# Performance work log

Hardware: AMD Instinct MI355X
Metric: run time of the kernel (lower is better)

The kernel has to match this reference:

```python
import jax, jax.numpy as jnp
import numpy as np

B, L, D = 2, 2048, 1024
H = 16          # num_heads
HD = D // H     # head_dim = 64
NEG_INF = jnp.float32(-1e30)


def setup_inputs() -> dict:
    key = jax.random.key(0)
    ks = jax.random.split(key, 10)
    s = 1.0 / np.sqrt(D)
    return {
        "x": jax.random.normal(ks[0], (B, L, D), dtype=jnp.float32),
        "Wq": jax.random.normal(ks[1], (D, D), dtype=jnp.float32) * s,
        "bq": jnp.zeros((D,), jnp.float32),
        "Wk": jax.random.normal(ks[2], (D, D), dtype=jnp.float32) * s,
        "bk": jnp.zeros((D,), jnp.float32),
        "Wv": jax.random.normal(ks[3], (D, D), dtype=jnp.float32) * s,
        "bv": jnp.zeros((D,), jnp.float32),
        "Wo": jax.random.normal(ks[4], (D, D), dtype=jnp.float32) * s,
        "bo": jnp.zeros((D,), jnp.float32),
        "local_scale": jnp.ones((1,), jnp.float32),
        "global_scale": jnp.ones((1,), jnp.float32),
    }


def reference(x, Wq, bq, Wk, bk, Wv, bv, Wo, bo, local_scale, global_scale):
    # projections -> [B, H, L, HD]
    def proj(W, b):
        return (x @ W + b).reshape(B, L, H, HD).transpose(0, 2, 1, 3)
    Q, K, V = proj(Wq, bq), proj(Wk, bk), proj(Wv, bv)
    lh = H // 2
    inv_sqrt = 1.0 / jnp.sqrt(jnp.float32(HD))

    # local (causal) heads
    scores_l = jnp.einsum("bhqd,bhkd->bhqk", Q[:, :lh], K[:, :lh]) * inv_sqrt
    causal = jnp.tril(jnp.ones((L, L), dtype=bool))  # keep lower triangle
    scores_l = jnp.where(causal, scores_l * local_scale, NEG_INF)
    attn_local = jax.nn.softmax(scores_l, axis=-1)
    out_local = jnp.einsum("bhqk,bhkd->bhqd", attn_local, V[:, :lh])

    # global (full) heads
    scores_g = jnp.einsum("bhqd,bhkd->bhqk", Q[:, lh:], K[:, lh:]) * inv_sqrt
    attn_global = jax.nn.softmax(scores_g * global_scale, axis=-1)
    out_global = jnp.einsum("bhqk,bhkd->bhqd", attn_global, V[:, lh:])

    out = jnp.concatenate([out_local, out_global], axis=1)  # [B,H,L,HD]
    out = out.transpose(0, 2, 1, 3).reshape(B, L, D)
    out = out @ Wo + bo
    return (out, attn_local, attn_global)
```

## Files before the change

### kernel.cpp

```cpp
#include <hip/hip_runtime.h>
#include <hip/hip_bf16.h>

#define B 2
#define L 2048
#define D 1024
#define H 16
#define HD 64
#define LH 8
#define NEG_INF -1e30f

typedef __hip_bfloat16 bf16;
typedef unsigned short ushort_t;
typedef short bf16x8 __attribute__((ext_vector_type(8)));
typedef unsigned short us8 __attribute__((ext_vector_type(8)));
typedef float f32x4 __attribute__((ext_vector_type(4)));

#define MFMA16(a, b, c) __builtin_amdgcn_mfma_f32_16x16x32_bf16((a), (b), (c), 0, 0, 0)

#if defined(__has_builtin)
#if __has_builtin(__builtin_amdgcn_global_load_lds)
#define HAVE_GLOAD_LDS 1
#endif
#endif

template<typename T> struct IsF32;
template<> struct IsF32<float> { static constexpr int value = 1; };
template<> struct IsF32<bf16>  { static constexpr int value = 0; };

__device__ __forceinline__ float ldf(const float* p, size_t i) { return p[i]; }
__device__ __forceinline__ float ldf(const bf16* p, size_t i) { return __bfloat162float(p[i]); }

__device__ __forceinline__ float4 ld4(const float* p, size_t i) {
  return *reinterpret_cast<const float4*>(p + i);
}
__device__ __forceinline__ float4 ld4(const bf16* p, size_t i) {
  ushort4 u = *reinterpret_cast<const ushort4*>(p + i);
  float4 f;
  f.x = __uint_as_float(((unsigned)u.x) << 16);
  f.y = __uint_as_float(((unsigned)u.y) << 16);
  f.z = __uint_as_float(((unsigned)u.z) << 16);
  f.w = __uint_as_float(((unsigned)u.w) << 16);
  return f;
}
__device__ __forceinline__ ushort_t bfh(float v) {
  bf16 h = __float2bfloat16(v);
  return *reinterpret_cast<ushort_t*>(&h);
}
__device__ __forceinline__ float bf2f(ushort_t u) {
  return __uint_as_float(((unsigned)u) << 16);
}
__device__ __forceinline__ void stf(float* p, size_t i, float v) { p[i] = v; }
__device__ __forceinline__ void stf(bf16* p, size_t i, float v) { p[i] = __float2bfloat16(v); }

__device__ __forceinline__ int swz(int row, int slot) {
  return row * 64 + (((slot ^ (row & 7)) & 7) << 3);
}
__device__ __forceinline__ int swzc(int row, int c) {
  return row * 64 + (((((c >> 3) ^ row) & 7) << 3) | (c & 7));
}

#if defined(HAVE_GLOAD_LDS)
__device__ __forceinline__ void gload_lds16(const ushort_t* src, ushort_t* dst) {
  __builtin_amdgcn_global_load_lds(
      (const __attribute__((address_space(1))) unsigned int*)src,
      (__attribute__((address_space(3))) unsigned int*)dst, 16, 0, 0);
}
#endif

__device__ __forceinline__ void stage64(const ushort_t* g, size_t gstride,
                                        ushort_t* lds, int w, int ln) {
  #pragma unroll
  for (int c = 0; c < 2; ++c) {
    const int row = 16 * w + 8 * c + (ln >> 3);
    const int slot = ((ln & 7) ^ row) & 7;
    const ushort_t* src = g + (size_t)row * gstride + slot * 8;
#if defined(HAVE_GLOAD_LDS)
    gload_lds16(src, lds + (size_t)(16 * w + 8 * c) * 64);
#else
    *reinterpret_cast<uint4*>(&lds[row * 64 + (ln & 7) * 8]) =
        *reinterpret_cast<const uint4*>(src);
#endif
  }
}

__device__ __forceinline__ void stage128(const ushort_t* g, ushort_t* lds,
                                         int w, int ln) {
  #pragma unroll
  for (int c = 0; c < 4; ++c) {
    const int row = 32 * w + 8 * c + (ln >> 3);
    const int slot = ((ln & 7) ^ row) & 7;
    const ushort_t* src = g + (size_t)row * 1024 + slot * 8;
#if defined(HAVE_GLOAD_LDS)
    gload_lds16(src, lds + (size_t)(32 * w + 8 * c) * 64);
#else
    *reinterpret_cast<uint4*>(&lds[row * 64 + (ln & 7) * 8]) =
        *reinterpret_cast<const uint4*>(src);
#endif
  }
}

__global__ void detect_dtype_kernel(const unsigned short* __restrict__ x,
                                    int* __restrict__ flag) {
  int bad = 0;
  for (int i = threadIdx.x; i < 1024; i += 64) {
    if (((x[i] >> 7) & 0xFF) >= 170) bad = 1;
  }
  unsigned long long m = __ballot(bad);
  if (threadIdx.x == 0) *flag = (m != 0ULL) ? 1 : 0;
}

__global__ __launch_bounds__(256)
void split_f32_kernel(const int* __restrict__ flag, int want,
                      const float* __restrict__ in,
                      ushort_t* __restrict__ hp, ushort_t* __restrict__ lp, int n4) {
  if (*flag != want) return;
  int i = blockIdx.x * 256 + threadIdx.x;
  const int stride = gridDim.x * 256;
  for (; i < n4; i += stride) {
    float4 v = *reinterpret_cast<const float4*>(in + 4 * (size_t)i);
    ushort4 h, l;
    h.x = bfh(v.x); l.x = bfh(v.x - bf2f(h.x));
    h.y = bfh(v.y); l.y = bfh(v.y - bf2f(h.y));
    h.z = bfh(v.z); l.z = bfh(v.z - bf2f(h.z));
    h.w = bfh(v.w); l.w = bfh(v.w - bf2f(h.w));
    *reinterpret_cast<ushort4*>(hp + 4 * (size_t)i) = h;
    *reinterpret_cast<ushort4*>(lp + 4 * (size_t)i) = l;
  }
}

template<typename T>
__global__ __launch_bounds__(256)
void transW_kernel(const int* __restrict__ flag,
                   const T* __restrict__ W0, const T* __restrict__ W1,
                   const T* __restrict__ W2, const T* __restrict__ W3,
                   ushort_t* __restrict__ base, ushort_t* __restrict__ baseWo,
                   int lo_upto) {
  if (*flag != IsF32<T>::value) return;
  const int z = blockIdx.z;
  const T* W = z == 0 ? W0 : (z == 1 ? W1 : (z == 2 ? W2 : W3));
  ushort_t* hp = (z < 3) ? (base + (size_t)z * 2097152) : baseWo;
  ushort_t* lp = hp + 1048576;
  const bool wl_ = IsF32<T>::value && (z < lo_upto);
  __shared__ float ts[64][69];
  const int k0 = blockIdx.x * 64, n0 = blockIdx.y * 64;
  const int t = threadIdx.x;
  #pragma unroll
  for (int p = 0; p < 4; ++p) {
    int r = p * 16 + (t >> 4);
    int c = (t & 15) * 4;
    float4 v = ld4(W, (size_t)(k0 + r) * D + n0 + c);
    ts[r][c] = v.x; ts[r][c + 1] = v.y; ts[r][c + 2] = v.z; ts[r][c + 3] = v.w;
  }
  __syncthreads();
  #pragma unroll
  for (int p = 0; p < 4; ++p) {
    int n = p * 16 + (t >> 4);
    int k4 = (t & 15) * 4;
    ushort4 h, l;
    float a0 = ts[k4][n], a1 = ts[k4 + 1][n], a2 = ts[k4 + 2][n], a3 = ts[k4 + 3][n];
    h.x = bfh(a0); l.x = bfh(a0 - bf2f(h.x));
    h.y = bfh(a1); l.y = bfh(a1 - bf2f(h.y));
    h.z = bfh(a2); l.z = bfh(a2 - bf2f(h.z));
    h.w = bfh(a3); l.w = bfh(a3 - bf2f(h.w));
    size_t o = (size_t)(n0 + n) * D + k0 + k4;
    *reinterpret_cast<ushort4*>(hp + o) = h;
    if (wl_) *reinterpret_cast<ushort4*>(lp + o) = l;
  }
}

template<typename T, int NSA, bool FULL>
__global__ __launch_bounds__(256, FULL ? 3 : 4)
void gemm_kernel(const int* __restrict__ flag,
                 const ushort_t* __restrict__ xA, const ushort_t* __restrict__ xAl,
                 const ushort_t* __restrict__ aoh,
                 const ushort_t* __restrict__ wbase, const ushort_t* __restrict__ woT,
                 const T* __restrict__ bq, const T* __restrict__ bk,
                 const T* __restrict__ bv, const T* __restrict__ bo,
                 ushort_t* __restrict__ qh, ushort_t* __restrict__ ql,
                 ushort_t* __restrict__ kh, ushort_t* __restrict__ kl,
                 ushort_t* __restrict__ vth, T* __restrict__ out0, int zfix) {
  if (*flag != IsF32<T>::value) return;
  const int cpx = gridDim.x >> 3;
  const int swzid = ((int)blockIdx.x & 7) * cpx + ((int)blockIdx.x >> 3);
  const int mtile = swzid & 31;
  const int ntile = (swzid >> 5) & 15;
  const int z = (zfix >= 0) ? zfix : (swzid >> 9);
  const int m0 = mtile * 128, n0 = ntile * 64;

  const bool isOut = (z == 3);
  const ushort_t* Ah = isOut ? aoh : xA;
  const ushort_t* wh = isOut ? woT : (wbase + (size_t)z * 2097152);
  const ushort_t* wl = wh + 1048576;

  constexpr int LDSUS = FULL ? 24576 : 12288;
  __shared__ ushort_t lds[LDSUS];
  ushort_t* AsH = lds;
  ushort_t* BsH = lds + 8192;
  ushort_t* AsL = FULL ? (lds + 12288) : nullptr;
  ushort_t* BsL = FULL ? (lds + 20480) : nullptr;

  const int ln = threadIdx.x & 63, w = threadIdx.x >> 6;
  const int m = ln & 15, hi = ln >> 4;

  f32x4 acc[2][4] = {};

  for (int k0 = 0; k0 < 1024; k0 += 64) {
    stage128(Ah + (size_t)m0 * 1024 + k0, AsH, w, ln);
    stage64(wh + (size_t)n0 * 1024 + k0, 1024, BsH, w, ln);
    if constexpr (FULL) {
      stage128(xAl + (size_t)m0 * 1024 + k0, AsL, w, ln);
      stage64(wl + (size_t)n0 * 1024 + k0, 1024, BsL, w, ln);
    }
    __syncthreads();
    #pragma unroll
    for (int kc = 0; kc < 2; ++kc) {
      bf16x8 a_h[2], b_h[4];
      #pragma unroll
      for (int f = 0; f < 2; ++f)
        a_h[f] = *reinterpret_cast<const bf16x8*>(&AsH[swz(w * 32 + f * 16 + m, kc * 4 + hi)]);
      #pragma unroll
      for (int f = 0; f < 4; ++f)
        b_h[f] = *reinterpret_cast<const bf16x8*>(&BsH[swz(f * 16 + m, kc * 4 + hi)]);
      #pragma unroll
      for (int fr = 0; fr < 2; ++fr)
        #pragma unroll
        for (int fc = 0; fc < 4; ++fc)
          acc[fr][fc] = MFMA16(a_h[fr], b_h[fc], acc[fr][fc]);
      if constexpr (FULL) {
        bf16x8 a_l[2], b_l[4];
        #pragma unroll
        for (int f = 0; f < 2; ++f)
          a_l[f] = *reinterpret_cast<const bf16x8*>(&AsL[swz(w * 32 + f * 16 + m, kc * 4 + hi)]);
        #pragma unroll
        for (int f = 0; f < 4; ++f)
          b_l[f] = *reinterpret_cast<const bf16x8*>(&BsL[swz(f * 16 + m, kc * 4 + hi)]);
        #pragma unroll
        for (int fr = 0; fr < 2; ++fr)
          #pragma unroll
          for (int fc = 0; fc < 4; ++fc) {
            acc[fr][fc] = MFMA16(a_h[fr], b_l[fc], acc[fr][fc]);
            acc[fr][fc] = MFMA16(a_l[fr], b_h[fc], acc[fr][fc]);
          }
      }
    }
    __syncthreads();
  }

  #pragma unroll
  for (int fc = 0; fc < 4; ++fc) {
    const int col = n0 + fc * 16 + m;
    if (isOut) {
      const float bv_ = ldf(bo, (size_t)col);
      #pragma unroll
      for (int fr = 0; fr < 2; ++fr)
        #pragma unroll
        for (int r = 0; r < 4; ++r) {
          const int tok = m0 + w * 32 + fr * 16 + 4 * hi + r;
          stf(out0, (size_t)tok * D + col, acc[fr][fc][r] + bv_);
        }
    } else if (z == 2) {
      const int hh = col >> 6, d = col & 63;
      const float bv_ = ldf(bv, (size_t)col);
      #pragma unroll
      for (int fr = 0; fr < 2; ++fr) {
        const int tok0 = m0 + w * 32 + fr * 16 + 4 * hi;
        const int bb = tok0 >> 11, ll = tok0 & (L - 1);
        ushort4 hv;
        hv.x = bfh(acc[fr][fc][0] + bv_);
        hv.y = bfh(acc[fr][fc][1] + bv_);
        hv.z = bfh(acc[fr][fc][2] + bv_);
        hv.w = bfh(acc[fr][fc][3] + bv_);
        *reinterpret_cast<ushort4*>(
            &vth[((size_t)(bb * H + hh) * HD + d) * L + ll]) = hv;
      }
    } else {
      const int hh = col >> 6, d = col & 63;
      const float bv_ = ldf(z == 0 ? bq : bk, (size_t)col);
      ushort_t* oh = z == 0 ? qh : kh;
      ushort_t* ol = z == 0 ? ql : kl;
      #pragma unroll
      for (int fr = 0; fr < 2; ++fr)
        #pragma unroll
        for (int r = 0; r < 4; ++r) {
          const int tok = m0 + w * 32 + fr * 16 + 4 * hi + r;
          const int bb = tok >> 11, ll = tok & (L - 1);
          const float v = acc[fr][fc][r] + bv_;
          const size_t o = ((size_t)(bb * H + hh) * L + ll) * HD + d;
          const ushort_t hu = bfh(v);
          oh[o] = hu; ol[o] = bfh(v - bf2f(hu));
        }
    }
  }
}

template<typename T>
__global__ __launch_bounds__(256, 2)
void attn_kernel(const int* __restrict__ flag,
                 const ushort_t* __restrict__ Qh_g, const ushort_t* __restrict__ Ql_g,
                 const ushort_t* __restrict__ Kh_g, const ushort_t* __restrict__ Kl_g,
                 const ushort_t* __restrict__ Vth_g,
                 const T* __restrict__ lsp, const T* __restrict__ gsp,
                 T* __restrict__ attn_l, T* __restrict__ attn_g,
                 ushort_t* __restrict__ AOh) {
  if (*flag != IsF32<T>::value) return;
  const int bid = blockIdx.x;
  const int xcd = bid & 7, slot = bid >> 3;
  const int bhg = xcd + 8 * (slot >> 5);
  const int strip_raw = slot & 31;
  const int bb = bhg >> 4, h = bhg & 15;
  const bool is_local = h < LH;
  const int strip = is_local ? (31 - strip_raw) : strip_raw;
  const int q0 = strip * 64;
  const int ln = threadIdx.x & 63, w = threadIdx.x >> 6;
  const int m = ln & 15, hi = ln >> 4;

  const float cscale =
      (is_local ? ldf(lsp, (size_t)0) : ldf(gsp, (size_t)0)) * 0.125f;
  const size_t bh_off = ((size_t)bb * H + h) * L * HD;
  const ushort_t* Qhb = Qh_g + bh_off;
  const ushort_t* Qlb = Ql_g + bh_off;
  const ushort_t* Khb = Kh_g + bh_off;
  const ushort_t* Klb = Kl_g + bh_off;
  const ushort_t* Vhb = Vth_g + bh_off;

  __shared__ ushort_t KsH[2][4096], KsL[2][4096], VsH[2][4096], Ps[4096];

  bf16x8 qfh[2], qfl[2];
  {
    const size_t qb = (size_t)(q0 + 16 * w + m) * HD + hi * 8;
    qfh[0] = *reinterpret_cast<const bf16x8*>(Qhb + qb);
    qfh[1] = *reinterpret_cast<const bf16x8*>(Qhb + qb + 32);
    qfl[0] = *reinterpret_cast<const bf16x8*>(Qlb + qb);
    qfl[1] = *reinterpret_cast<const bf16x8*>(Qlb + qb + 32);
  }

  float m_ = NEG_INF, l_ = 0.f;
  const int nkt = is_local ? (strip + 1) : (L / 64);
  T* aout = is_local ? attn_l : attn_g;
  const size_t arow0 =
      ((size_t)(bb * LH + (is_local ? h : h - LH)) * L + q0) * L;

  stage64(Khb, HD, KsH[0], w, ln);
  __syncthreads();
  for (int kt = 0; kt < nkt; ++kt) {
    const int cur = kt & 1;
    if (kt + 1 < nkt)
      stage64(Khb + (size_t)((kt + 1) * 64) * HD, HD, KsH[cur ^ 1], w, ln);

    f32x4 s[4] = {};
    __builtin_amdgcn_s_setprio(1);
    #pragma unroll
    for (int nt = 0; nt < 4; ++nt) {
      #pragma unroll
      for (int kc = 0; kc < 2; ++kc) {
        bf16x8 kbh = *reinterpret_cast<const bf16x8*>(&KsH[cur][swz(nt * 16 + m, kc * 4 + hi)]);
        s[nt] = MFMA16(kbh, qfh[kc], s[nt]);
      }
    }
    __builtin_amdgcn_s_setprio(0);

    const bool dg = is_local && (kt == strip);
    #pragma unroll
    for (int nt = 0; nt < 4; ++nt)
      #pragma unroll
      for (int r = 0; r < 4; ++r) {
        float v = s[nt][r] * cscale;
        if (dg && (nt * 16 + 4 * hi + r > 16 * w + m)) v = NEG_INF;
        s[nt][r] = v;
      }

    float tm = NEG_INF;
    #pragma unroll
    for (int nt = 0; nt < 4; ++nt)
      #pragma unroll
      for (int r = 0; r < 4; ++r) tm = fmaxf(tm, s[nt][r]);
    tm = fmaxf(tm, __shfl_xor(tm, 16, 64));
    tm = fmaxf(tm, __shfl_xor(tm, 32, 64));
    const float mn = fmaxf(m_, tm);
    float sum = 0.f;
    #pragma unroll
    for (int nt = 0; nt < 4; ++nt)
      #pragma unroll
      for (int r = 0; r < 4; ++r) sum += __expf(s[nt][r] - mn);
    sum += __shfl_xor(sum, 16, 64);
    sum += __shfl_xor(sum, 32, 64);
    l_ = l_ * __expf(m_ - mn) + sum;
    m_ = mn;
    __syncthreads();
  }

  const float invl = 1.0f / l_;
  f32x4 o_[4] = {};

  stage64(Khb, HD, KsH[0], w, ln);
  stage64(Klb, HD, KsL[0], w, ln);
  stage64(Vhb, L, VsH[0], w, ln);
  __syncthreads();
  for (int kt = 0; kt < nkt; ++kt) {
    const int cur = kt & 1;
    if (kt + 1 < nkt) {
      stage64(Khb + (size_t)((kt + 1) * 64) * HD, HD, KsH[cur ^ 1], w, ln);
      stage64(Klb + (size_t)((kt + 1) * 64) * HD, HD, KsL[cur ^ 1], w, ln);
      stage64(Vhb + (size_t)((kt + 1) * 64), L, VsH[cur ^ 1], w, ln);
    }

    f32x4 s[4] = {};
    __builtin_amdgcn_s_setprio(1);
    #pragma unroll
    for (int nt = 0; nt < 4; ++nt) {
      #pragma unroll
      for (int kc = 0; kc < 2; ++kc) {
        bf16x8 kbh = *reinterpret_cast<const bf16x8*>(&KsH[cur][swz(nt * 16 + m, kc * 4 + hi)]);
        bf16x8 kbl = *reinterpret_cast<const bf16x8*>(&KsL[cur][swz(nt * 16 + m, kc * 4 + hi)]);
        s[nt] = MFMA16(kbh, qfh[kc], s[nt]);
        s[nt] = MFMA16(kbl, qfh[kc], s[nt]);
        s[nt] = MFMA16(kbh, qfl[kc], s[nt]);
      }
    }
    __builtin_amdgcn_s_setprio(0);

    const bool dg = is_local && (kt == strip);
    #pragma unroll
    for (int nt = 0; nt < 4; ++nt) {
      float v0 = s[nt][0] * cscale, v1 = s[nt][1] * cscale;
      float v2 = s[nt][2] * cscale, v3 = s[nt][3] * cscale;
      if (dg) {
        const int kbq = nt * 16 + 4 * hi, qq = 16 * w + m;
        if (kbq + 0 > qq) v0 = NEG_INF;
        if (kbq + 1 > qq) v1 = NEG_INF;
        if (kbq + 2 > qq) v2 = NEG_INF;
        if (kbq + 3 > qq) v3 = NEG_INF;
      }
      ushort4 pk;
      pk.x = bfh(__expf(v0 - m_) * invl);
      pk.y = bfh(__expf(v1 - m_) * invl);
      pk.z = bfh(__expf(v2 - m_) * invl);
      pk.w = bfh(__expf(v3 - m_) * invl);
      *reinterpret_cast<ushort4*>(&Ps[swzc(16 * w + m, nt * 16 + 4 * hi)]) = pk;
    }

    __builtin_amdgcn_s_setprio(1);
    bf16x8 pf0 = *reinterpret_cast<const bf16x8*>(&Ps[swz(16 * w + m, hi)]);
    bf16x8 pf1 = *reinterpret_cast<const bf16x8*>(&Ps[swz(16 * w + m, 4 + hi)]);
    #pragma unroll
    for (int dt = 0; dt < 4; ++dt) {
      bf16x8 vf0 = *reinterpret_cast<const bf16x8*>(&VsH[cur][swz(dt * 16 + m, hi)]);
      bf16x8 vf1 = *reinterpret_cast<const bf16x8*>(&VsH[cur][swz(dt * 16 + m, 4 + hi)]);
      o_[dt] = MFMA16(pf0, vf0, o_[dt]);
      o_[dt] = MFMA16(pf1, vf1, o_[dt]);
    }
    __builtin_amdgcn_s_setprio(0);

    {
      const int pr = 16 * w + (ln >> 2);
      const int cs = (ln & 3) * 2;
      us8 v0 = *reinterpret_cast<const us8*>(&Ps[swz(pr, cs)]);
      us8 v1 = *reinterpret_cast<const us8*>(&Ps[swz(pr, cs + 1)]);
      const size_t gi = arow0 + (size_t)pr * L + (size_t)(kt * 64 + (ln & 3) * 16);
      if constexpr (IsF32<T>::value) {
        float* dst = (float*)aout + gi;
        *reinterpret_cast<float4*>(dst + 0) =
            make_float4(bf2f(v0[0]), bf2f(v0[1]), bf2f(v0[2]), bf2f(v0[3]));
        *reinterpret_cast<float4*>(dst + 4) =
            make_float4(bf2f(v0[4]), bf2f(v0[5]), bf2f(v0[6]), bf2f(v0[7]));
        *reinterpret_cast<float4*>(dst + 8) =
            make_float4(bf2f(v1[0]), bf2f(v1[1]), bf2f(v1[2]), bf2f(v1[3]));
        *reinterpret_cast<float4*>(dst + 12) =
            make_float4(bf2f(v1[4]), bf2f(v1[5]), bf2f(v1[6]), bf2f(v1[7]));
      } else {
        bf16* dst = (bf16*)aout + gi;
        *reinterpret_cast<uint4*>(dst + 0) = *reinterpret_cast<const uint4*>(&v0);
        *reinterpret_cast<uint4*>(dst + 8) = *reinterpret_cast<const uint4*>(&v1);
      }
    }
    __syncthreads();
  }

  if (is_local) {
    const int pr = 16 * w + (ln >> 2);
    const size_t rbase = arow0 + (size_t)pr * L;
    for (int c = nkt * 64 + (ln & 3) * 16; c < L; c += 64) {
      if constexpr (IsF32<T>::value) {
        float* dst = (float*)aout + rbase + c;
        const float4 z4 = make_float4(0.f, 0.f, 0.f, 0.f);
        *reinterpret_cast<float4*>(dst + 0) = z4;
        *reinterpret_cast<float4*>(dst + 4) = z4;
        *reinterpret_cast<float4*>(dst + 8) = z4;
        *reinterpret_cast<float4*>(dst + 12) = z4;
      } else {
        bf16* dst = (bf16*)aout + rbase + c;
        const uint4 z4 = make_uint4(0u, 0u, 0u, 0u);
        *reinterpret_cast<uint4*>(dst + 0) = z4;
        *reinterpret_cast<uint4*>(dst + 8) = z4;
      }
    }
  }

  #pragma unroll
  for (int dt = 0; dt < 4; ++dt)
    #pragma unroll
    for (int r = 0; r < 4; ++r)
      AOh[((size_t)bb * L + q0 + 16 * w + 4 * hi + r) * D + h * HD + dt * 16 + m] =
          bfh(o_[dt][r]);
}

template<typename T>
static void launch_path(void* const* d_in, void* d_out, void* d_ws, hipStream_t stream) {
  const int want = IsF32<T>::value;
  const int* flag = (const int*)d_ws;
  ushort_t* Qh  = (ushort_t*)((char*)d_ws + 256);
  ushort_t* Ql  = Qh + 4194304;
  ushort_t* Kh  = Ql + 4194304;
  ushort_t* Kl  = Kh + 4194304;
  ushort_t* Vth = Kl + 4194304;
  ushort_t* AOh = Vth + 4194304;
  ushort_t* Woth = AOh + 4194304;

  const T* x  = (const T*)d_in[0];
  const T* Wq = (const T*)d_in[1];
  const T* bq = (const T*)d_in[2];
  const T* Wk = (const T*)d_in[3];
  const T* bk = (const T*)d_in[4];
  const T* Wv = (const T*)d_in[5];
  const T* bv = (const T*)d_in[6];
  const T* Wo = (const T*)d_in[7];
  const T* bo = (const T*)d_in[8];
  const T* ls = (const T*)d_in[9];
  const T* gs = (const T*)d_in[10];

  T* out0   = (T*)d_out;
  T* attn_l = out0 + (size_t)B * L * D;
  T* attn_g = attn_l + (size_t)B * LH * L * L;
  ushort_t* xh  = (ushort_t*)attn_g;
  ushort_t* xl  = xh + 4194304;
  ushort_t* Wt3 = xh + 8388608;

  constexpr int NSA = IsF32<T>::value ? 2 : 1;

  if constexpr (IsF32<T>::value)
    split_f32_kernel<<<1024, 256, 0, stream>>>(flag, want, (const float*)x, xh, xl, 1048576);
  transW_kernel<T><<<dim3(16, 16, 4), 256, 0, stream>>>(
      flag, Wq, Wk, Wv, Wo, Wt3, Woth, 2);
  const ushort_t* xA = IsF32<T>::value ? xh : (const ushort_t*)x;

  if constexpr (IsF32<T>::value) {
    gemm_kernel<T, NSA, true><<<1024, 256, 0, stream>>>(
        flag, xA, xl, AOh, Wt3, Woth, bq, bk, bv, bo,
        Qh, Ql, Kh, Kl, Vth, out0, -1);
    gemm_kernel<T, NSA, false><<<512, 256, 0, stream>>>(
        flag, xA, xl, AOh, Wt3, Woth, bq, bk, bv, bo,
        Qh, Ql, Kh, Kl, Vth, out0, 2);
  } else {
    gemm_kernel<T, NSA, false><<<1536, 256, 0, stream>>>(
        flag, xA, xl, AOh, Wt3, Woth, bq, bk, bv, bo,
        Qh, Ql, Kh, Kl, Vth, out0, -1);
  }
  attn_kernel<T><<<1024, 256, 0, stream>>>(
      flag, Qh, Ql, Kh, Kl, Vth, ls, gs, attn_l, attn_g, AOh);
  gemm_kernel<T, NSA, false><<<512, 256, 0, stream>>>(
      flag, xA, xl, AOh, Wt3, Woth, bq, bk, bv, bo,
      Qh, Ql, Kh, Kl, Vth, out0, 3);
}

extern "C" void kernel_launch(void* const* d_in, const int* in_sizes, int n_in,
                              void* d_out, int out_size, void* d_ws, size_t ws_size,
                              hipStream_t stream) {
  int* flag = (int*)d_ws;
  detect_dtype_kernel<<<1, 64, 0, stream>>>((const unsigned short*)d_in[0], flag);
  launch_path<float>(d_in, d_out, d_ws, stream);
  launch_path<bf16>(d_in, d_out, d_ws, stream);
}
```

Baseline: 966.9 us.

## Drop split-bf16 precision in projections, double-buffer GEMM, single-buffer V in attention

Removes the hi/lo bf16 split of x and the Q/K weights, so the Q/K projection GEMMs run a single bf16 MFMA pass and all projections use one unified GEMM launch. The GEMM k-loop gains double-buffered LDS staging with raised MFMA wave priority. The attention kernel single-buffers V with an extra barrier, freeing LDS so occupancy can rise to 3 blocks. The trade-off is lower projection accuracy for Q/K, which could affect attention-probability tolerance, and the V load is no longer prefetched.

Result: faster. 927.3 us (-4.1%).

```diff
diff --git a/kernel.cpp b/kernel.cpp
--- a/kernel.cpp
+++ b/kernel.cpp
@@ -110,21 +110,17 @@
 }
 
 __global__ __launch_bounds__(256)
-void split_f32_kernel(const int* __restrict__ flag, int want,
-                      const float* __restrict__ in,
-                      ushort_t* __restrict__ hp, ushort_t* __restrict__ lp, int n4) {
+void cast_f32_kernel(const int* __restrict__ flag, int want,
+                     const float* __restrict__ in,
+                     ushort_t* __restrict__ hp, int n4) {
   if (*flag != want) return;
   int i = blockIdx.x * 256 + threadIdx.x;
   const int stride = gridDim.x * 256;
   for (; i < n4; i += stride) {
     float4 v = *reinterpret_cast<const float4*>(in + 4 * (size_t)i);
-    ushort4 h, l;
-    h.x = bfh(v.x); l.x = bfh(v.x - bf2f(h.x));
-    h.y = bfh(v.y); l.y = bfh(v.y - bf2f(h.y));
-    h.z = bfh(v.z); l.z = bfh(v.z - bf2f(h.z));
-    h.w = bfh(v.w); l.w = bfh(v.w - bf2f(h.w));
+    ushort4 h;
+    h.x = bfh(v.x); h.y = bfh(v.y); h.z = bfh(v.z); h.w = bfh(v.w);
     *reinterpret_cast<ushort4*>(hp + 4 * (size_t)i) = h;
-    *reinterpret_cast<ushort4*>(lp + 4 * (size_t)i) = l;
   }
 }
 
@@ -133,14 +129,11 @@
 void transW_kernel(const int* __restrict__ flag,
                    const T* __restrict__ W0, const T* __restrict__ W1,
                    const T* __restrict__ W2, const T* __restrict__ W3,
-                   ushort_t* __restrict__ base, ushort_t* __restrict__ baseWo,
-                   int lo_upto) {
+                   ushort_t* __restrict__ base, ushort_t* __restrict__ baseWo) {
   if (*flag != IsF32<T>::value) return;
   const int z = blockIdx.z;
   const T* W = z == 0 ? W0 : (z == 1 ? W1 : (z == 2 ? W2 : W3));
   ushort_t* hp = (z < 3) ? (base + (size_t)z * 2097152) : baseWo;
-  ushort_t* lp = hp + 1048576;
-  const bool wl_ = IsF32<T>::value && (z < lo_upto);
   __shared__ float ts[64][69];
   const int k0 = blockIdx.x * 64, n0 = blockIdx.y * 64;
   const int t = threadIdx.x;
@@ -156,23 +149,19 @@
   for (int p = 0; p < 4; ++p) {
     int n = p * 16 + (t >> 4);
     int k4 = (t & 15) * 4;
-    ushort4 h, l;
-    float a0 = ts[k4][n], a1 = ts[k4 + 1][n], a2 = ts[k4 + 2][n], a3 = ts[k4 + 3][n];
-    h.x = bfh(a0); l.x = bfh(a0 - bf2f(h.x));
-    h.y = bfh(a1); l.y = bfh(a1 - bf2f(h.y));
-    h.z = bfh(a2); l.z = bfh(a2 - bf2f(h.z));
-    h.w = bfh(a3); l.w = bfh(a3 - bf2f(h.w));
-    size_t o = (size_t)(n0 + n) * D + k0 + k4;
-    *reinterpret_cast<ushort4*>(hp + o) = h;
-    if (wl_) *reinterpret_cast<ushort4*>(lp + o) = l;
-  }
-}
-
-template<typename T, int NSA, bool FULL>
-__global__ __launch_bounds__(256, FULL ? 3 : 4)
+    ushort4 h;
+    h.x = bfh(ts[k4][n]);
+    h.y = bfh(ts[k4 + 1][n]);
+    h.z = bfh(ts[k4 + 2][n]);
+    h.w = bfh(ts[k4 + 3][n]);
+    *reinterpret_cast<ushort4*>(&hp[(size_t)(n0 + n) * D + k0 + k4]) = h;
+  }
+}
+
+template<typename T>
+__global__ __launch_bounds__(256, 3)
 void gemm_kernel(const int* __restrict__ flag,
-                 const ushort_t* __restrict__ xA, const ushort_t* __restrict__ xAl,
-                 const ushort_t* __restrict__ aoh,
+                 const ushort_t* __restrict__ xA, const ushort_t* __restrict__ aoh,
                  const ushort_t* __restrict__ wbase, const ushort_t* __restrict__ woT,
                  const T* __restrict__ bq, const T* __restrict__ bk,
                  const T* __restrict__ bv, const T* __restrict__ bo,
@@ -190,59 +179,40 @@
   const bool isOut = (z == 3);
   const ushort_t* Ah = isOut ? aoh : xA;
   const ushort_t* wh = isOut ? woT : (wbase + (size_t)z * 2097152);
-  const ushort_t* wl = wh + 1048576;
-
-  constexpr int LDSUS = FULL ? 24576 : 12288;
-  __shared__ ushort_t lds[LDSUS];
-  ushort_t* AsH = lds;
-  ushort_t* BsH = lds + 8192;
-  ushort_t* AsL = FULL ? (lds + 12288) : nullptr;
-  ushort_t* BsL = FULL ? (lds + 20480) : nullptr;
+
+  __shared__ ushort_t As[2][8192], Bs[2][4096];
 
   const int ln = threadIdx.x & 63, w = threadIdx.x >> 6;
   const int m = ln & 15, hi = ln >> 4;
 
   f32x4 acc[2][4] = {};
 
-  for (int k0 = 0; k0 < 1024; k0 += 64) {
-    stage128(Ah + (size_t)m0 * 1024 + k0, AsH, w, ln);
-    stage64(wh + (size_t)n0 * 1024 + k0, 1024, BsH, w, ln);
-    if constexpr (FULL) {
-      stage128(xAl + (size_t)m0 * 1024 + k0, AsL, w, ln);
-      stage64(wl + (size_t)n0 * 1024 + k0, 1024, BsL, w, ln);
-    }
-    __syncthreads();
+  stage128(Ah + (size_t)m0 * 1024, As[0], w, ln);
+  stage64(wh + (size_t)n0 * 1024, 1024, Bs[0], w, ln);
+  __syncthreads();
+  for (int step = 0; step < 16; ++step) {
+    const int cur = step & 1;
+    if (step < 15) {
+      stage128(Ah + (size_t)m0 * 1024 + (step + 1) * 64, As[cur ^ 1], w, ln);
+      stage64(wh + (size_t)n0 * 1024 + (step + 1) * 64, 1024, Bs[cur ^ 1], w, ln);
+    }
+    __builtin_amdgcn_s_setprio(1);
     #pragma unroll
     for (int kc = 0; kc < 2; ++kc) {
       bf16x8 a_h[2], b_h[4];
       #pragma unroll
       for (int f = 0; f < 2; ++f)
-        a_h[f] = *reinterpret_cast<const bf16x8*>(&AsH[swz(w * 32 + f * 16 + m, kc * 4 + hi)]);
+        a_h[f] = *reinterpret_cast<const bf16x8*>(&As[cur][swz(w * 32 + f * 16 + m, kc * 4 + hi)]);
       #pragma unroll
       for (int f = 0; f < 4; ++f)
-        b_h[f] = *reinterpret_cast<const bf16x8*>(&BsH[swz(f * 16 + m, kc * 4 + hi)]);
+        b_h[f] = *reinterpret_cast<const bf16x8*>(&Bs[cur][swz(f * 16 + m, kc * 4 + hi)]);
       #pragma unroll
       for (int fr = 0; fr < 2; ++fr)
         #pragma unroll
         for (int fc = 0; fc < 4; ++fc)
           acc[fr][fc] = MFMA16(a_h[fr], b_h[fc], acc[fr][fc]);
-      if constexpr (FULL) {
-        bf16x8 a_l[2], b_l[4];
-        #pragma unroll
-        for (int f = 0; f < 2; ++f)
-          a_l[f] = *reinterpret_cast<const bf16x8*>(&AsL[swz(w * 32 + f * 16 + m, kc * 4 + hi)]);
-        #pragma unroll
-        for (int f = 0; f < 4; ++f)
-          b_l[f] = *reinterpret_cast<const bf16x8*>(&BsL[swz(f * 16 + m, kc * 4 + hi)]);
-        #pragma unroll
-        for (int fr = 0; fr < 2; ++fr)
-          #pragma unroll
-          for (int fc = 0; fc < 4; ++fc) {
-            acc[fr][fc] = MFMA16(a_h[fr], b_l[fc], acc[fr][fc]);
-            acc[fr][fc] = MFMA16(a_l[fr], b_h[fc], acc[fr][fc]);
-          }
-      }
-    }
+    }
+    __builtin_amdgcn_s_setprio(0);
     __syncthreads();
   }
 
@@ -294,7 +264,7 @@
 }
 
 template<typename T>
-__global__ __launch_bounds__(256, 2)
+__global__ __launch_bounds__(256, 3)
 void attn_kernel(const int* __restrict__ flag,
                  const ushort_t* __restrict__ Qh_g, const ushort_t* __restrict__ Ql_g,
                  const ushort_t* __restrict__ Kh_g, const ushort_t* __restrict__ Kl_g,
@@ -323,7 +293,7 @@
   const ushort_t* Klb = Kl_g + bh_off;
   const ushort_t* Vhb = Vth_g + bh_off;
 
-  __shared__ ushort_t KsH[2][4096], KsL[2][4096], VsH[2][4096], Ps[4096];
+  __shared__ ushort_t KsH[2][4096], KsL[2][4096], VsH[4096], Ps[4096];
 
   bf16x8 qfh[2], qfl[2];
   {
@@ -394,15 +364,14 @@
 
   stage64(Khb, HD, KsH[0], w, ln);
   stage64(Klb, HD, KsL[0], w, ln);
-  stage64(Vhb, L, VsH[0], w, ln);
   __syncthreads();
   for (int kt = 0; kt < nkt; ++kt) {
     const int cur = kt & 1;
     if (kt + 1 < nkt) {
       stage64(Khb + (size_t)((kt + 1) * 64) * HD, HD, KsH[cur ^ 1], w, ln);
       stage64(Klb + (size_t)((kt + 1) * 64) * HD, HD, KsL[cur ^ 1], w, ln);
-      stage64(Vhb + (size_t)((kt + 1) * 64), L, VsH[cur ^ 1], w, ln);
-    }
+    }
+    stage64(Vhb + (size_t)(kt * 64), L, VsH, w, ln);
 
     f32x4 s[4] = {};
     __builtin_amdgcn_s_setprio(1);
@@ -438,14 +407,15 @@
       pk.w = bfh(__expf(v3 - m_) * invl);
       *reinterpret_cast<ushort4*>(&Ps[swzc(16 * w + m, nt * 16 + 4 * hi)]) = pk;
     }
+    __syncthreads();
 
     __builtin_amdgcn_s_setprio(1);
     bf16x8 pf0 = *reinterpret_cast<const bf16x8*>(&Ps[swz(16 * w + m, hi)]);
     bf16x8 pf1 = *reinterpret_cast<const bf16x8*>(&Ps[swz(16 * w + m, 4 + hi)]);
     #pragma unroll
     for (int dt = 0; dt < 4; ++dt) {
-      bf16x8 vf0 = *reinterpret_cast<const bf16x8*>(&VsH[cur][swz(dt * 16 + m, hi)]);
-      bf16x8 vf1 = *reinterpret_cast<const bf16x8*>(&VsH[cur][swz(dt * 16 + m, 4 + hi)]);
+      bf16x8 vf0 = *reinterpret_cast<const bf16x8*>(&VsH[swz(dt * 16 + m, hi)]);
+      bf16x8 vf1 = *reinterpret_cast<const bf16x8*>(&VsH[swz(dt * 16 + m, 4 + hi)]);
       o_[dt] = MFMA16(pf0, vf0, o_[dt]);
       o_[dt] = MFMA16(pf1, vf1, o_[dt]);
     }
@@ -532,33 +502,21 @@
   T* attn_l = out0 + (size_t)B * L * D;
   T* attn_g = attn_l + (size_t)B * LH * L * L;
   ushort_t* xh  = (ushort_t*)attn_g;
-  ushort_t* xl  = xh + 4194304;
-  ushort_t* Wt3 = xh + 8388608;
-
-  constexpr int NSA = IsF32<T>::value ? 2 : 1;
+  ushort_t* Wt3 = xh + 4194304;
 
   if constexpr (IsF32<T>::value)
-    split_f32_kernel<<<1024, 256, 0, stream>>>(flag, want, (const float*)x, xh, xl, 1048576);
+    cast_f32_kernel<<<1024, 256, 0, stream>>>(flag, want, (const float*)x, xh, 1048576);
   transW_kernel<T><<<dim3(16, 16, 4), 256, 0, stream>>>(
-      flag, Wq, Wk, Wv, Wo, Wt3, Woth, 2);
+      flag, Wq, Wk, Wv, Wo, Wt3, Woth);
   const ushort_t* xA = IsF32<T>::value ? xh : (const ushort_t*)x;
 
-  if constexpr (IsF32<T>::value) {
-    gemm_kernel<T, NSA, true><<<1024, 256, 0, stream>>>(
-        flag, xA, xl, AOh, Wt3, Woth, bq, bk, bv, bo,
-        Qh, Ql, Kh, Kl, Vth, out0, -1);
-    gemm_kernel<T, NSA, false><<<512, 256, 0, stream>>>(
-        flag, xA, xl, AOh, Wt3, Woth, bq, bk, bv, bo,
-        Qh, Ql, Kh, Kl, Vth, out0, 2);
-  } else {
-    gemm_kernel<T, NSA, false><<<1536, 256, 0, stream>>>(
-        flag, xA, xl, AOh, Wt3, Woth, bq, bk, bv, bo,
-        Qh, Ql, Kh, Kl, Vth, out0, -1);
-  }
+  gemm_kernel<T><<<1536, 256, 0, stream>>>(
+      flag, xA, AOh, Wt3, Woth, bq, bk, bv, bo,
+      Qh, Ql, Kh, Kl, Vth, out0, -1);
   attn_kernel<T><<<1024, 256, 0, stream>>>(
       flag, Qh, Ql, Kh, Kl, Vth, ls, gs, attn_l, attn_g, AOh);
-  gemm_kernel<T, NSA, false><<<512, 256, 0, stream>>>(
-      flag, xA, xl, AOh, Wt3, Woth, bq, bk, bv, bo,
+  gemm_kernel<T><<<512, 256, 0, stream>>>(
+      flag, xA, AOh, Wt3, Woth, bq, bk, bv, bo,
       Qh, Ql, Kh, Kl, Vth, out0, 3);
 }
 
```
